# Kernel tuning notes

Hardware: AMD Instinct MI355X
Metric: run time of the kernel (lower is better)

## Reference

```python
import jax, jax.numpy as jnp
import numpy as np

B, EMB, ARRAY = 4096, 512, 2
KW = KH = KC = 8
OC = 16                      # output_channel per branch
RED = OC * 2                 # SE hidden width
NUM_REL = 500
FC_IN = 3 * OC * KH * KW * KC  # 24576, flattened concat of 3 branches


def _make_chequer_perm():
    # Deterministic replication of MSLE.get_chequer_perm (perm=1).
    rng = np.random.RandomState(0)
    ent_perm = rng.permutation(EMB * (ARRAY - 1))
    rel_perm = rng.permutation(EMB)
    idxs, ei, ri = [], 0, 0
    for i in range(KC):
        for j in range(KH):
            for k in range(KW):
                for m in range(ARRAY):
                    if (i + j) % ARRAY == m:
                        idxs.append(int(rel_perm[ri]) + EMB * (ARRAY - 1)); ri += 1
                    else:
                        idxs.append(int(ent_perm[ei])); ei += 1
    return jnp.asarray(np.asarray(idxs, dtype=np.int32))


def setup_inputs() -> dict:
    key = jax.random.key(0)
    ks = jax.random.split(key, 12)
    n = lambda k, shape, s=0.05: jax.random.normal(k, shape, jnp.float32) * s
    f1_dim = ARRAY * OC * 1 * 1 * ARRAY        # (1,1,2) kernels
    f3_dim = ARRAY * OC * 1 * ARRAY * ARRAY    # (1,2,2) kernels
    f5_dim = ARRAY * OC * ARRAY * ARRAY * ARRAY  # (2,2,2) kernels
    z = lambda shape: jnp.zeros(shape, jnp.float32)
    o = lambda shape: jnp.ones(shape, jnp.float32)
    return {
        "concat_input": jax.random.normal(ks[0], (B, EMB * ARRAY), jnp.float32),
        "rel": jax.random.randint(ks[1], (B,), 0, NUM_REL),
        "chequer_perm": _make_chequer_perm(),
        "f1_table": n(ks[2], (NUM_REL, f1_dim)),
        "f3_table": n(ks[3], (NUM_REL, f3_dim)),
        "f5_table": n(ks[4], (NUM_REL, f5_dim)),
        "bn0_g": o((ARRAY,)), "bn0_b": z((ARRAY,)),
        "bn1_g": o((OC,)), "bn1_b": z((OC,)),
        "bn2_g": o((OC,)), "bn2_b": z((OC,)),
        "bn3_g": o((OC,)), "bn3_b": z((OC,)),
        "att_Wsq": n(ks[5], (OC, RED)), "att_bsq": z((RED,)),
        "att_W1": n(ks[6], (RED, OC)), "att_b1": z((OC,)),
        "att_W2": n(ks[7], (RED, OC)), "att_b2": z((OC,)),
        "att_W3": n(ks[8], (RED, OC)), "att_b3": z((OC,)),
        "fc_W": n(ks[9], (FC_IN, EMB), 0.01), "fc_b": z((EMB,)),
    }


def _bn(x, g, b, eps=1e-5):
    # BatchNorm3d, training-mode batch statistics over (N, D, H, W).
    m = x.mean(axis=(0, 2, 3, 4), keepdims=True)
    v = x.var(axis=(0, 2, 3, 4), keepdims=True)
    sh = (1, -1, 1, 1, 1)
    return (x - m) * jax.lax.rsqrt(v + eps) * g.reshape(sh) + b.reshape(sh)


def _per_sample_conv(x, w):
    # x: (B, Cin, D, H, W); w: (B, Cout, Cin, kd, kh, kw). 'same' padding,
    # even kernels pad the extra element at the high end (torch padding='same').
    conv1 = lambda xb, wb: jax.lax.conv_general_dilated(
        xb[None], wb, (1, 1, 1), 'SAME',
        dimension_numbers=('NCDHW', 'OIDHW', 'NCDHW'))[0]
    return jax.vmap(conv1)(x, w)


def reference(concat_input, rel, chequer_perm, f1_table, f3_table, f5_table,
              bn0_g, bn0_b, bn1_g, bn1_b, bn2_g, bn2_b, bn3_g, bn3_b,
              att_Wsq, att_bsq, att_W1, att_b1, att_W2, att_b2, att_W3, att_b3,
              fc_W, fc_b):
    b = concat_input.shape[0]
    # Chequered interleave of entity / relation embedding dims.
    x = concat_input[:, chequer_perm].reshape(b, ARRAY, KW, KH, KC)
    x = _bn(x, bn0_g, bn0_b)  # dropout = identity (eval)
    # Per-sample dynamic filters from relation embeddings.
    f1 = f1_table[rel].reshape(b, OC, ARRAY, 1, 1, ARRAY)
    f3 = f3_table[rel].reshape(b, OC, ARRAY, 1, ARRAY, ARRAY)
    f5 = f5_table[rel].reshape(b, OC, ARRAY, ARRAY, ARRAY, ARRAY)
    x1 = _bn(_per_sample_conv(x, f1), bn1_g, bn1_b)
    x3 = _bn(_per_sample_conv(x, f3), bn2_g, bn2_b)
    x5 = _bn(_per_sample_conv(x, f5), bn3_g, bn3_b)
    xs = x1 + x3 + x5
    # SE-style 3D attention: global pool -> shared squeeze -> 3 sigmoid gates.
    pooled = xs.mean(axis=(2, 3, 4))                       # (B, OC)
    zq = jax.nn.relu(pooled @ att_Wsq + att_bsq)           # (B, RED)
    gate = lambda W, bb: jax.nn.sigmoid(zq @ W + bb)[:, :, None, None, None]
    x1 = x1 * gate(att_W1, att_b1)
    x3 = x3 * gate(att_W2, att_b2)
    x5 = x5 * gate(att_W3, att_b3)
    out = jax.nn.relu(jnp.concatenate([x1, x3, x5], axis=1))
    out = out.reshape(b, -1)                               # (B, FC_IN)
    return out @ fc_W + fc_b                               # (B, EMB)
```

## Files before the change

### kernel.cpp

```cpp
#include <hip/hip_runtime.h>
#include <hip/hip_bf16.h>
#include <stdint.h>

typedef short s16x8 __attribute__((ext_vector_type(8)));
typedef short s16x4 __attribute__((ext_vector_type(4)));
typedef float f32x4 __attribute__((ext_vector_type(4)));

#define NB 4096
#define KTOT 24576
#define NOUT 512
#define NCH 48

__device__ __forceinline__ short f2bf(float f){
  union { float f; uint32_t u; } x; x.f = f;
  uint32_t r = (x.u + 0x7FFFu + ((x.u >> 16) & 1u)) >> 16;
  return (short)r;
}
__device__ __forceinline__ float bf2f(short s){
  union { uint32_t u; float f; } x; x.u = ((uint32_t)(uint16_t)s) << 16;
  return x.f;
}
__device__ __forceinline__ short f2bf_fast(float x){
  union { __hip_bfloat16 h; short s; } c; c.h = __float2bfloat16(x); return c.s;
}

#define GLOAD16(g, l) __builtin_amdgcn_global_load_lds( \
  (const __attribute__((address_space(1))) void*)(g), \
  (__attribute__((address_space(3))) void*)(l), 16, 0, 0)

__global__ __launch_bounds__(256) void k_colmap(const int* __restrict__ perm,
                                                int* __restrict__ chmap,
                                                float* __restrict__ statf){
  int q = blockIdx.x * 256 + threadIdx.x;
  if (q < 1024) chmap[perm[q]] = q >> 9;
  if (blockIdx.x == 0 && threadIdx.x < 4) statf[threadIdx.x] = 0.f;
}

__global__ __launch_bounds__(256) void k_bn0(const float* __restrict__ concat,
                                             const int* __restrict__ chmap,
                                             float* __restrict__ statf){
  int t = threadIdx.x;
  float s0=0,q0=0,s1=0,q1=0;
  for (int idx = blockIdx.x*256 + t; idx < NB*1024; idx += gridDim.x*256){
    float v = concat[idx];
    int ch = chmap[idx & 1023];
    if (ch){ s1 += v; q1 += v*v; } else { s0 += v; q0 += v*v; }
  }
  #pragma unroll
  for (int m=1;m<64;m<<=1){
    s0 += __shfl_xor(s0,m); q0 += __shfl_xor(q0,m);
    s1 += __shfl_xor(s1,m); q1 += __shfl_xor(q1,m);
  }
  __shared__ float lb[4][4];
  int wid = t>>6, lane = t&63;
  if (lane==0){ lb[wid][0]=s0; lb[wid][1]=q0; lb[wid][2]=s1; lb[wid][3]=q1; }
  __syncthreads();
  if (t==0){
    float a0=0,a1=0,a2=0,a3=0;
    #pragma unroll
    for (int w=0;w<4;w++){ a0+=lb[w][0]; a1+=lb[w][1]; a2+=lb[w][2]; a3+=lb[w][3]; }
    atomicAdd(&statf[0],a0); atomicAdd(&statf[1],a1);
    atomicAdd(&statf[2],a2); atomicAdd(&statf[3],a3);
  }
}

__global__ __launch_bounds__(256) void k_wcast(const float* __restrict__ fcW,
                                               short* __restrict__ wT){
  __shared__ float tile[64][65];
  int bid = blockIdx.x;
  int kb = (bid % 384) * 64;
  int nb = (bid / 384) * 64;
  int t = threadIdx.x;
  #pragma unroll
  for (int i=0;i<16;i++){
    int r = i*4 + (t>>6), c = t & 63;
    tile[r][c] = fcW[(size_t)(kb + r)*NOUT + nb + c];
  }
  __syncthreads();
  #pragma unroll
  for (int i=0;i<16;i++){
    int n = i*4 + (t>>6), k = t & 63;
    wT[(size_t)(nb + n)*KTOT + kb + k] = f2bf(tile[k][n]);
  }
}

__global__ __launch_bounds__(256) void k_conv(
    const float* __restrict__ concat, const int* __restrict__ perm,
    const int* __restrict__ rel,
    const float* __restrict__ f1t, const float* __restrict__ f3t,
    const float* __restrict__ f5t,
    const float* __restrict__ statf,
    const float* __restrict__ bn0g, const float* __restrict__ bn0b,
    short* __restrict__ raw, float* __restrict__ psum, float* __restrict__ psq)
{
  const int b = blockIdx.x;
  const int t = threadIdx.x;
  __shared__ float xn[2*9*9*9];
  __shared__ float filt[448];
  for (int i=t;i<1458;i+=256) xn[i]=0.f;
  int r = rel[b];
  for (int i=t;i<448;i+=256){
    float v;
    if (i < 64)       v = f1t[r*64 + i];
    else if (i < 192) v = f3t[r*128 + (i-64)];
    else              v = f5t[r*256 + (i-192)];
    filt[i]=v;
  }
  __syncthreads();
  const float n0inv = 1.f/(4096.f*512.f);
  float m0 = statf[0]*n0inv, e0 = statf[1]*n0inv;
  float m1 = statf[2]*n0inv, e1 = statf[3]*n0inv;
  float sc0 = bn0g[0]*rsqrtf(e0-m0*m0+1e-5f), sh0 = bn0b[0]-m0*sc0;
  float sc1 = bn0g[1]*rsqrtf(e1-m1*m1+1e-5f), sh1 = bn0b[1]-m1*sc1;
  for (int q=t;q<1024;q+=256){
    int col = perm[q];
    float v = concat[(size_t)b*1024 + col];
    int ch = q>>9, s = q & 511;
    int d = s>>6, h=(s>>3)&7, w=s&7;
    xn[ch*729 + d*81 + h*9 + w] = ch ? v*sc1+sh1 : v*sc0+sh0;
  }
  __syncthreads();

  const int wid = t>>6, lane = t&63;
  const int d = lane>>3, h = lane&7;
  float r00[9], r01[9], r10[9], r11[9], r20[9], r21[9], r30[9], r31[9];
  #pragma unroll
  for (int w9=0;w9<9;w9++){
    int base0 = d*81 + h*9 + w9;
    int base1 = d*81 + (h+1)*9 + w9;
    int base2 = (d+1)*81 + h*9 + w9;
    int base3 = (d+1)*81 + (h+1)*9 + w9;
    r00[w9]=xn[base0];      r01[w9]=xn[729+base0];
    r10[w9]=xn[base1];      r11[w9]=xn[729+base1];
    r20[w9]=xn[base2];      r21[w9]=xn[729+base2];
    r30[w9]=xn[base3];      r31[w9]=xn[729+base3];
  }
  const size_t rawbase = (size_t)b*KTOT;

  auto finish = [&](int c, const float* v){
    float s=0,q=0;
    #pragma unroll
    for (int p=0;p<8;p++){ s += v[p]; q += v[p]*v[p]; }
    #pragma unroll
    for (int m=1;m<64;m<<=1){ s += __shfl_xor(s,m); q += __shfl_xor(q,m); }
    if (lane==0){ psum[c*NB+b]=s; psq[c*NB+b]=q; }
    s16x8 pk;
    #pragma unroll
    for (int p=0;p<8;p++) pk[p] = f2bf(v[p]);
    *reinterpret_cast<s16x8*>(raw + rawbase + (size_t)c*512 + lane*8) = pk;
  };

  #pragma unroll
  for (int i=0;i<4;i++){
    int oc = wid + 4*i;
    float c0=filt[oc*4+0], c1=filt[oc*4+1], c2=filt[oc*4+2], c3=filt[oc*4+3];
    float v[8];
    #pragma unroll
    for (int p=0;p<8;p++)
      v[p] = c0*r00[p]+c1*r00[p+1]+c2*r01[p]+c3*r01[p+1];
    finish(oc, v);
  }
  #pragma unroll
  for (int i=0;i<4;i++){
    int oc = wid + 4*i;
    const float* cf = &filt[64 + oc*8];
    float v[8];
    #pragma unroll
    for (int p=0;p<8;p++)
      v[p] = cf[0]*r00[p]+cf[1]*r00[p+1]+cf[2]*r10[p]+cf[3]*r10[p+1]
           + cf[4]*r01[p]+cf[5]*r01[p+1]+cf[6]*r11[p]+cf[7]*r11[p+1];
    finish(16+oc, v);
  }
  #pragma unroll
  for (int i=0;i<4;i++){
    int oc = wid + 4*i;
    const float* cf = &filt[192 + oc*16];
    float v[8];
    #pragma unroll
    for (int p=0;p<8;p++)
      v[p] = cf[0]*r00[p] +cf[1]*r00[p+1] +cf[2]*r10[p] +cf[3]*r10[p+1]
           + cf[4]*r20[p] +cf[5]*r20[p+1] +cf[6]*r30[p] +cf[7]*r30[p+1]
           + cf[8]*r01[p] +cf[9]*r01[p+1] +cf[10]*r11[p]+cf[11]*r11[p+1]
           + cf[12]*r21[p]+cf[13]*r21[p+1]+cf[14]*r31[p]+cf[15]*r31[p+1];
    finish(32+oc, v);
  }
}

__global__ __launch_bounds__(256) void k_bnstats(
    const float* __restrict__ psum, const float* __restrict__ psq,
    const float* __restrict__ bn1g, const float* __restrict__ bn1b,
    const float* __restrict__ bn2g, const float* __restrict__ bn2b,
    const float* __restrict__ bn3g, const float* __restrict__ bn3b,
    float* __restrict__ statf)
{
  int c = blockIdx.x, t = threadIdx.x;
  float s=0,q=0;
  for (int b=t;b<NB;b+=256){ s += psum[c*NB+b]; q += psq[c*NB+b]; }
  #pragma unroll
  for (int m=1;m<64;m<<=1){ s += __shfl_xor(s,m); q += __shfl_xor(q,m); }
  __shared__ float lb[4][2];
  int wid = t>>6, lane = t&63;
  if (lane==0){ lb[wid][0]=s; lb[wid][1]=q; }
  __syncthreads();
  if (t==0){
    s = lb[0][0]+lb[1][0]+lb[2][0]+lb[3][0];
    q = lb[0][1]+lb[1][1]+lb[2][1]+lb[3][1];
    float n = 4096.f*512.f;
    float mean = s/n, var = q/n - mean*mean;
    const float* g  = c<16 ? bn1g : (c<32 ? bn2g : bn3g);
    const float* bb = c<16 ? bn1b : (c<32 ? bn2b : bn3b);
    int oc = c & 15;
    float sc = g[oc]*rsqrtf(var + 1e-5f);
    statf[16+c] = sc;
    statf[64+c] = bb[oc] - mean*sc;
  }
}

__global__ __launch_bounds__(64) void k_se(
    const float* __restrict__ psum, const float* __restrict__ statf,
    const float* __restrict__ Wsq, const float* __restrict__ bsq,
    const float* __restrict__ W1, const float* __restrict__ b1,
    const float* __restrict__ W2, const float* __restrict__ b2,
    const float* __restrict__ W3, const float* __restrict__ b3,
    float* __restrict__ gates)
{
  int b = blockIdx.x, lane = threadIdx.x;
  __shared__ float pooled[16];
  __shared__ float zq[32];
  if (lane < 16){
    float p = 0.f;
    #pragma unroll
    for (int br=0;br<3;br++){
      int c = br*16 + lane;
      p += psum[c*NB+b]*(1.f/512.f)*statf[16+c] + statf[64+c];
    }
    pooled[lane] = p;
  }
  __syncthreads();
  if (lane < 32){
    float z = bsq[lane];
    #pragma unroll
    for (int oc=0;oc<16;oc++) z += pooled[oc]*Wsq[oc*32+lane];
    zq[lane] = fmaxf(z, 0.f);
  }
  __syncthreads();
  if (lane < 48){
    int br = lane>>4, oc = lane&15;
    const float* W  = br==0 ? W1 : (br==1 ? W2 : W3);
    const float* bb = br==0 ? b1 : (br==1 ? b2 : b3);
    float g = bb[oc];
    #pragma unroll
    for (int r2=0;r2<32;r2++) g += zq[r2]*W[r2*16+oc];
    gates[lane*NB + b] = 1.f/(1.f + expf(-g));
  }
}

__global__ __launch_bounds__(512, 4) void k_gemm(
    const short* __restrict__ raw, const short* __restrict__ wT,
    const float* __restrict__ scale, const float* __restrict__ shift,
    const float* __restrict__ gates, short* __restrict__ partials)
{
  const int t = threadIdx.x;
  const int bid = blockIdx.x;
  const int sk = bid >> 6, rem = bid & 63;
  const int nblk = rem >> 5, mblk = rem & 31;
  const int b0 = mblk*128, n0 = nblk*256;
  const int kb0 = sk*3072;

  __shared__ short As[2][128][40];
  __shared__ short Ws[2][8192];

  const int wid = t>>6, lane = t&63;

  const int arow = t>>2, acol = (t&3)<<3;
  const short* aptr = raw + (size_t)(b0+arow)*KTOT + kb0 + acol;

  const int nl0 = wid*32 + (lane>>2);
  const int nl1 = nl0 + 16;
  const int sl0 = (lane&3) ^ ((nl0>>1)&3);
  const int sl1 = (lane&3) ^ ((nl1>>1)&3);
  const short* wp0 = wT + (size_t)(n0+nl0)*KTOT + kb0 + sl0*8;
  const short* wp1 = wT + (size_t)(n0+nl1)*KTOT + kb0 + sl1*8;
  const int ldsw0 = wid*1024;
  const int ldsw1 = wid*1024 + 512;

  f32x4 acc[4][4];
  #pragma unroll
  for (int m=0;m<4;m++)
    #pragma unroll
    for (int n=0;n<4;n++){ f32x4 z = {0.f,0.f,0.f,0.f}; acc[m][n]=z; }

  const int wr = (wid>>2)*64, wc = (wid&3)*64;
  const int fr = lane&15, fkq = lane>>4;

  int wroff[4];
  #pragma unroll
  for (int n=0;n<4;n++){
    int r = wc + n*16 + fr;
    wroff[n] = r*64 + ((fkq ^ ((r>>1)&3))<<4);
  }

  GLOAD16(wp0, &Ws[0][ldsw0]);
  GLOAD16(wp1, &Ws[0][ldsw1]);
  s16x8 aReg = *reinterpret_cast<const s16x8*>(aptr);
  int ch = kb0 >> 9;
  float g = gates[ch*NB + b0 + arow];
  float scg = scale[ch]*g, shg = shift[ch]*g;
  {
    s16x8 av;
    #pragma unroll
    for (int j=0;j<8;j++)
      av[j] = f2bf_fast(fmaxf(bf2f(aReg[j])*scg + shg, 0.f));
    *reinterpret_cast<s16x8*>(&As[0][arow][acol]) = av;
  }
  __syncthreads();

  int cur = 0;
  for (int step=0; step<96; ++step){
    const int nxt = cur ^ 1;
    if (step < 95){
      const int ko = (step+1)*32;
      GLOAD16(wp0 + ko, &Ws[nxt][ldsw0]);
      GLOAD16(wp1 + ko, &Ws[nxt][ldsw1]);
      aReg = *reinterpret_cast<const s16x8*>(aptr + ko);
      int nch = (kb0 + ko) >> 9;
      if (nch != ch){
        ch = nch;
        g = gates[ch*NB + b0 + arow];
        scg = scale[ch]*g; shg = shift[ch]*g;
      }
    }
    {
      const short* asb = &As[cur][0][0];
      const char*  wsb = (const char*)&Ws[cur][0];
      s16x8 af[4], bfm[4];
      #pragma unroll
      for (int m=0;m<4;m++)
        af[m] = *reinterpret_cast<const s16x8*>(asb + (wr + m*16 + fr)*40 + fkq*8);
      #pragma unroll
      for (int n=0;n<4;n++)
        bfm[n] = *reinterpret_cast<const s16x8*>(wsb + wroff[n]);
      #pragma unroll
      for (int m=0;m<4;m++)
        #pragma unroll
        for (int n=0;n<4;n++)
          acc[m][n] = __builtin_amdgcn_mfma_f32_16x16x32_bf16(af[m], bfm[n], acc[m][n], 0,0,0);
    }
    if (step < 95){
      s16x8 av;
      #pragma unroll
      for (int j=0;j<8;j++)
        av[j] = f2bf_fast(fmaxf(bf2f(aReg[j])*scg + shg, 0.f));
      *reinterpret_cast<s16x8*>(&As[nxt][arow][acol]) = av;
    }
    __syncthreads();
    cur = nxt;
  }

  short* pb = partials + (size_t)sk*NB*NOUT;
  #pragma unroll
  for (int m=0;m<4;m++){
    #pragma unroll
    for (int j=0;j<4;j++){
      int row = b0 + wr + m*16 + (lane>>4)*4 + j;
      short* prow = pb + (size_t)row*NOUT + n0 + wc + fr;
      #pragma unroll
      for (int n=0;n<4;n++) prow[n*16] = f2bf(acc[m][n][j]);
    }
  }
}

__global__ __launch_bounds__(256) void k_red(const short* __restrict__ partials,
                                             const float* __restrict__ fcb,
                                             float* __restrict__ out){
  int i = blockIdx.x*256 + threadIdx.x;
  int base = i*4;
  f32x4 v = *reinterpret_cast<const f32x4*>(fcb + (base & 511));
  #pragma unroll
  for (int sk=0;sk<8;sk++){
    s16x4 p = *reinterpret_cast<const s16x4*>(partials + (size_t)sk*2097152 + base);
    v[0] += bf2f(p[0]); v[1] += bf2f(p[1]);
    v[2] += bf2f(p[2]); v[3] += bf2f(p[3]);
  }
  *reinterpret_cast<f32x4*>(out + base) = v;
}

extern "C" void kernel_launch(void* const* d_in, const int* in_sizes, int n_in,
                              void* d_out, int out_size, void* d_ws, size_t ws_size,
                              hipStream_t stream) {
  const float* concat = (const float*)d_in[0];
  const int*   rel    = (const int*)  d_in[1];
  const int*   perm   = (const int*)  d_in[2];
  const float* f1t = (const float*)d_in[3];
  const float* f3t = (const float*)d_in[4];
  const float* f5t = (const float*)d_in[5];
  const float* bn0g=(const float*)d_in[6],  *bn0b=(const float*)d_in[7];
  const float* bn1g=(const float*)d_in[8],  *bn1b=(const float*)d_in[9];
  const float* bn2g=(const float*)d_in[10], *bn2b=(const float*)d_in[11];
  const float* bn3g=(const float*)d_in[12], *bn3b=(const float*)d_in[13];
  const float* Wsq=(const float*)d_in[14],  *bsq=(const float*)d_in[15];
  const float* W1=(const float*)d_in[16],   *b1=(const float*)d_in[17];
  const float* W2=(const float*)d_in[18],   *b2=(const float*)d_in[19];
  const float* W3=(const float*)d_in[20],   *b3=(const float*)d_in[21];
  const float* fcW=(const float*)d_in[22],  *fcb=(const float*)d_in[23];
  float* out = (float*)d_out;
  char* ws = (char*)d_ws;

  const size_t off_raw  = 0;
  const size_t off_wT   = 201326592;
  const size_t off_part = 226492416;
  const size_t off_psum = 260046848;
  const size_t off_psq  = 260833280;
  const size_t off_gate = 261619712;
  const size_t off_stat = 262406144;
  const size_t off_chm  = 262406656;
  const size_t need     = off_chm + 4096;
  if (ws_size < need) return;

  short* raw      = (short*)(ws + off_raw);
  short* wT       = (short*)(ws + off_wT);
  short* partials = (short*)(ws + off_part);
  float* psum     = (float*)(ws + off_psum);
  float* psq      = (float*)(ws + off_psq);
  float* gates    = (float*)(ws + off_gate);
  float* statf    = (float*)(ws + off_stat);
  int*   chmap    = (int*)  (ws + off_chm);

  k_colmap<<<4, 256, 0, stream>>>(perm, chmap, statf);
  k_bn0   <<<2048, 256, 0, stream>>>(concat, chmap, statf);
  k_wcast <<<3072, 256, 0, stream>>>(fcW, wT);
  k_conv  <<<4096, 256, 0, stream>>>(concat, perm, rel, f1t, f3t, f5t,
                                     statf, bn0g, bn0b, raw, psum, psq);
  k_bnstats<<<48, 256, 0, stream>>>(psum, psq, bn1g, bn1b, bn2g, bn2b,
                                    bn3g, bn3b, statf);
  k_se    <<<4096, 64, 0, stream>>>(psum, statf, Wsq, bsq, W1, b1, W2, b2,
                                    W3, b3, gates);
  k_gemm  <<<512, 512, 0, stream>>>(raw, wT, statf+16, statf+64, gates, partials);
  k_red   <<<2048, 256, 0, stream>>>(partials, fcb, out);
}
```

Before: 362.7 us.

## Hoist bn0 channel lookup, LDS-reduce conv stats, thread-per-sample SE, remap GEMM blocks

Several unrelated tweaks land together. k_bn0 loads the channel map once per thread, since the stride is a multiple of 1024. k_conv swaps the full 64-lane shuffle reduction for an 8-lane shuffle plus an LDS reduction, and uses the hardware bf16 conversion. k_se becomes one thread per sample over 16 blocks instead of 4096 tiny blocks. k_gemm reorders the block index so the split-K slices sharing an output tile are adjacent, which may change L2 reuse of the activation and weight tiles.

```diff
diff --git a/kernel.cpp b/kernel.cpp
--- a/kernel.cpp
+++ b/kernel.cpp
@@ -40,10 +40,10 @@
                                              const int* __restrict__ chmap,
                                              float* __restrict__ statf){
   int t = threadIdx.x;
+  const int ch = chmap[(blockIdx.x*256 + t) & 1023];
   float s0=0,q0=0,s1=0,q1=0;
-  for (int idx = blockIdx.x*256 + t; idx < NB*1024; idx += gridDim.x*256){
+  for (int idx = blockIdx.x*256 + t; idx < NB*1024; idx += 2048*256){
     float v = concat[idx];
-    int ch = chmap[idx & 1023];
     if (ch){ s1 += v; q1 += v*v; } else { s0 += v; q0 += v*v; }
   }
   #pragma unroll
@@ -97,6 +97,7 @@
   const int t = threadIdx.x;
   __shared__ float xn[2*9*9*9];
   __shared__ float filt[448];
+  __shared__ float redS[48][9], redQ[48][9];
   for (int i=t;i<1458;i+=256) xn[i]=0.f;
   int r = rel[b];
   for (int i=t;i<448;i+=256){
@@ -141,12 +142,13 @@
     float s=0,q=0;
     #pragma unroll
     for (int p=0;p<8;p++){ s += v[p]; q += v[p]*v[p]; }
-    #pragma unroll
-    for (int m=1;m<64;m<<=1){ s += __shfl_xor(s,m); q += __shfl_xor(q,m); }
-    if (lane==0){ psum[c*NB+b]=s; psq[c*NB+b]=q; }
+    s += __shfl_xor(s,1); q += __shfl_xor(q,1);
+    s += __shfl_xor(s,2); q += __shfl_xor(q,2);
+    s += __shfl_xor(s,4); q += __shfl_xor(q,4);
+    if ((lane&7)==0){ redS[c][lane>>3]=s; redQ[c][lane>>3]=q; }
     s16x8 pk;
     #pragma unroll
-    for (int p=0;p<8;p++) pk[p] = f2bf(v[p]);
+    for (int p=0;p<8;p++) pk[p] = f2bf_fast(v[p]);
     *reinterpret_cast<s16x8*>(raw + rawbase + (size_t)c*512 + lane*8) = pk;
   };
 
@@ -183,6 +185,13 @@
            + cf[8]*r01[p] +cf[9]*r01[p+1] +cf[10]*r11[p]+cf[11]*r11[p+1]
            + cf[12]*r21[p]+cf[13]*r21[p+1]+cf[14]*r31[p]+cf[15]*r31[p+1];
     finish(32+oc, v);
+  }
+  __syncthreads();
+  if (t < 48){
+    float s=0,q=0;
+    #pragma unroll
+    for (int j=0;j<8;j++){ s += redS[t][j]; q += redQ[t][j]; }
+    psum[t*NB+b]=s; psq[t*NB+b]=q;
   }
 }
 
@@ -216,7 +225,7 @@
   }
 }
 
-__global__ __launch_bounds__(64) void k_se(
+__global__ __launch_bounds__(256) void k_se(
     const float* __restrict__ psum, const float* __restrict__ statf,
     const float* __restrict__ Wsq, const float* __restrict__ bsq,
     const float* __restrict__ W1, const float* __restrict__ b1,
@@ -224,34 +233,37 @@
     const float* __restrict__ W3, const float* __restrict__ b3,
     float* __restrict__ gates)
 {
-  int b = blockIdx.x, lane = threadIdx.x;
-  __shared__ float pooled[16];
-  __shared__ float zq[32];
-  if (lane < 16){
+  int b = blockIdx.x*256 + threadIdx.x;
+  float pooled[16];
+  #pragma unroll
+  for (int oc=0;oc<16;oc++){
     float p = 0.f;
     #pragma unroll
     for (int br=0;br<3;br++){
-      int c = br*16 + lane;
+      int c = br*16 + oc;
       p += psum[c*NB+b]*(1.f/512.f)*statf[16+c] + statf[64+c];
     }
-    pooled[lane] = p;
-  }
-  __syncthreads();
-  if (lane < 32){
-    float z = bsq[lane];
-    #pragma unroll
-    for (int oc=0;oc<16;oc++) z += pooled[oc]*Wsq[oc*32+lane];
-    zq[lane] = fmaxf(z, 0.f);
-  }
-  __syncthreads();
-  if (lane < 48){
-    int br = lane>>4, oc = lane&15;
+    pooled[oc] = p;
+  }
+  float zq[32];
+  #pragma unroll
+  for (int r2=0;r2<32;r2++){
+    float z = bsq[r2];
+    #pragma unroll
+    for (int oc=0;oc<16;oc++) z += pooled[oc]*Wsq[oc*32+r2];
+    zq[r2] = fmaxf(z, 0.f);
+  }
+  #pragma unroll
+  for (int br=0;br<3;br++){
     const float* W  = br==0 ? W1 : (br==1 ? W2 : W3);
     const float* bb = br==0 ? b1 : (br==1 ? b2 : b3);
-    float g = bb[oc];
-    #pragma unroll
-    for (int r2=0;r2<32;r2++) g += zq[r2]*W[r2*16+oc];
-    gates[lane*NB + b] = 1.f/(1.f + expf(-g));
+    #pragma unroll
+    for (int oc=0;oc<16;oc++){
+      float g = bb[oc];
+      #pragma unroll
+      for (int r2=0;r2<32;r2++) g += zq[r2]*W[r2*16+oc];
+      gates[(size_t)(br*16+oc)*NB + b] = 1.f/(1.f + expf(-g));
+    }
   }
 }
 
@@ -262,8 +274,8 @@
 {
   const int t = threadIdx.x;
   const int bid = blockIdx.x;
-  const int sk = bid >> 6, rem = bid & 63;
-  const int nblk = rem >> 5, mblk = rem & 31;
+  const int sk = bid & 7, rem = bid >> 3;
+  const int nblk = rem & 1, mblk = rem >> 1;
   const int b0 = mblk*128, n0 = nblk*256;
   const int kb0 = sk*3072;
 
@@ -365,7 +377,7 @@
       int row = b0 + wr + m*16 + (lane>>4)*4 + j;
       short* prow = pb + (size_t)row*NOUT + n0 + wc + fr;
       #pragma unroll
-      for (int n=0;n<4;n++) prow[n*16] = f2bf(acc[m][n][j]);
+      for (int n=0;n<4;n++) prow[n*16] = f2bf_fast(acc[m][n][j]);
     }
   }
 }
@@ -433,8 +445,8 @@
                                      statf, bn0g, bn0b, raw, psum, psq);
   k_bnstats<<<48, 256, 0, stream>>>(psum, psq, bn1g, bn1b, bn2g, bn2b,
                                     bn3g, bn3b, statf);
-  k_se    <<<4096, 64, 0, stream>>>(psum, statf, Wsq, bsq, W1, b1, W2, b2,
-                                    W3, b3, gates);
+  k_se    <<<16, 256, 0, stream>>>(psum, statf, Wsq, bsq, W1, b1, W2, b2,
+                                   W3, b3, gates);
   k_gemm  <<<512, 512, 0, stream>>>(raw, wT, statf+16, statf+64, gates, partials);
   k_red   <<<2048, 256, 0, stream>>>(partials, fcb, out);
 }
```

Result: slower. 390.4 us (+7.6%).
